# Performance work log

Measured on AMD Instinct MI355X. Metric: run time of the kernel, lower is better.

Reference implementation:

```python
import jax, jax.numpy as jnp
import numpy as np

N_HEAD = 16
RMS_EPS = 1.1920928955078125e-07  # torch F.rms_norm default eps = finfo(fp32).eps


def _rope_tables(seq_len, head_dim, dtype):
    steps = jnp.arange(seq_len, dtype=jnp.float32)
    rates = 10000.0 ** (-jnp.arange(0, head_dim, 2, dtype=jnp.float32) / head_dim)
    angles = jnp.outer(steps, rates)  # [S, D/2]
    return jnp.cos(angles).astype(dtype)[None, None], jnp.sin(angles).astype(dtype)[None, None]


def _apply_rotary(x, cos, sin):
    # interleaved RoPE: pairs (x[2i], x[2i+1]) rotated
    left = x[..., ::2]
    right = x[..., 1::2]
    lo = left * cos - right * sin
    ro = left * sin + right * cos
    return jnp.stack((lo, ro), axis=-1).reshape(x.shape)


def _rms_norm(x, eps=RMS_EPS):
    ms = jnp.mean(jnp.square(x), axis=-1, keepdims=True)
    return x * jax.lax.rsqrt(ms + eps)


def setup_inputs() -> dict:
    key = jax.random.key(0)
    k1, k2, k3 = jax.random.split(key, 3)
    B, S, E = 2, 2048, 2048
    x = jax.random.normal(k1, (B, S, E), dtype=jnp.float32)
    w_qkv = jax.random.normal(k2, (3 * E, E), dtype=jnp.float32) * (E ** -0.5)
    w_proj = jax.random.normal(k3, (E, E), dtype=jnp.float32) * (E ** -0.5)
    return {"x": x, "w_qkv": w_qkv, "w_proj": w_proj}


def reference(x, w_qkv, w_proj):
    B, S, E = x.shape
    H = N_HEAD
    D = E // H

    qkv = x @ w_qkv.T  # [B, S, 3E]
    q, k, v = jnp.split(qkv, 3, axis=-1)
    # [B, S, E] -> [B, H, S, D]
    q = q.reshape(B, S, H, D).transpose(0, 2, 1, 3)
    k = k.reshape(B, S, H, D).transpose(0, 2, 1, 3)
    v = v.reshape(B, S, H, D).transpose(0, 2, 1, 3)

    cos, sin = _rope_tables(S, D, x.dtype)  # [1,1,S,D/2]
    q = _apply_rotary(q, cos, sin)
    k = _apply_rotary(k, cos, sin)

    q = _rms_norm(q)
    k = _rms_norm(k)

    scale = 1.0 / jnp.sqrt(jnp.asarray(D, dtype=x.dtype))
    scores = jnp.einsum("bhqd,bhkd->bhqk", q, k) * scale  # [B,H,S,S]
    causal = jnp.tril(jnp.ones((S, S), dtype=bool))
    scores = jnp.where(causal[None, None], scores, jnp.asarray(-jnp.inf, dtype=scores.dtype))
    attn = jax.nn.softmax(scores, axis=-1)
    y = jnp.einsum("bhqk,bhkd->bhqd", attn, v)  # [B,H,S,D]
    y = y.transpose(0, 2, 1, 3).reshape(B, S, E)
    return y @ w_proj.T
```

## Files before the change

### kernel.cpp

```cpp
#include <hip/hip_runtime.h>

typedef unsigned short ushort_t;
using bf16x8 = __attribute__((ext_vector_type(8))) short;
using f32x4  = __attribute__((ext_vector_type(4))) float;

#define DEV static __device__ __forceinline__

DEV unsigned short f2bf(float f) {
  union { float f; unsigned u; } a; a.f = f;
  unsigned r = a.u + 0x7fffu + ((a.u >> 16) & 1u);
  return (unsigned short)(r >> 16);
}
DEV float bf2f(unsigned short u) {
  union { unsigned u; float f; } a; a.u = ((unsigned)u) << 16;
  return a.f;
}
DEV void load_lds16(const void* g, void* l) {
  __builtin_amdgcn_global_load_lds(
      (const __attribute__((address_space(1))) void*)g,
      (__attribute__((address_space(3))) void*)l, 16, 0, 0);
}

__global__ __launch_bounds__(256) void cast_kernel(
    const float* __restrict__ src, ushort_t* __restrict__ dst, int n4) {
  int i = blockIdx.x * 256 + threadIdx.x;
  if (i >= n4) return;
  float4 f = ((const float4*)src)[i];
  ushort4 o;
  o.x = f2bf(f.x); o.y = f2bf(f.y); o.z = f2bf(f.z); o.w = f2bf(f.w);
  ((ushort4*)dst)[i] = o;
}

__global__ __launch_bounds__(256) void rope_tables_kernel(float* __restrict__ tab) {
  int idx = blockIdx.x * 256 + threadIdx.x;
  int s = idx >> 6, i = idx & 63;
  float rate = exp2f(-13.287712379549449f * ((float)(2 * i) * (1.0f / 128.0f)));
  float ang = (float)s * rate;
  tab[idx * 2]     = cosf(ang);
  tab[idx * 2 + 1] = sinf(ang);
}

template<int BM, int BN, int OUTF32>
__global__ __launch_bounds__(256, 2) void gemm_bal(
    const ushort_t* __restrict__ A, const ushort_t* __restrict__ Bm,
    void* __restrict__ C, int M, int N, int K) {
  constexpr int MF   = BM / 32;
  constexpr int NF   = BN / 32;
  constexpr int NCA  = BM / 64;
  constexpr int NCB  = BN / 64;
  constexpr int NC   = NCA + NCB;
  constexpr int ABY  = BM * 64;
  constexpr int BUFB = (BM + BN) * 64;
  __shared__ __align__(16) char lds[2 * BUFB];

  const int nby = M / BM;
  const int nwg = nby * (N / BN);
  const int orig = blockIdx.x;
  const int wgid = (orig & 7) * (nwg >> 3) + (orig >> 3);
  const int bm = (wgid % nby) * BM;
  const int bn = (wgid / nby) * BN;

  const int tid = threadIdx.x;
  const int lane = tid & 63;
  const int wave = tid >> 6;
  const int ql = lane & 15, lk = lane >> 4;
  const int wm = wave >> 1, wn = wave & 1;

  f32x4 acc[MF][NF];
#pragma unroll
  for (int m = 0; m < MF; ++m)
#pragma unroll
    for (int n = 0; n < NF; ++n) acc[m][n] = (f32x4){0.f, 0.f, 0.f, 0.f};

  const int rin  = tid >> 2;
  const int sswz = ((tid & 3) ^ ((rin >> 1) & 3)) * 16;
  const size_t rb = (size_t)K * 2;
  const char* src[NC];
#pragma unroll
  for (int c = 0; c < NCA; ++c)
    src[c] = (const char*)A + (size_t)(bm + c * 64 + rin) * rb + sswz;
#pragma unroll
  for (int c = 0; c < NCB; ++c)
    src[NCA + c] = (const char*)Bm + (size_t)(bn + c * 64 + rin) * rb + sswz;
  char* const ldsc = (char*)lds;
  const int dT = tid * 16;

  int aOff[MF], bOff[NF];
#pragma unroll
  for (int m = 0; m < MF; ++m) {
    const int r = wm * (BM / 2) + m * 16 + ql;
    aOff[m] = r * 64 + ((lk ^ ((r >> 1) & 3)) * 16);
  }
#pragma unroll
  for (int n = 0; n < NF; ++n) {
    const int r = wn * (BN / 2) + n * 16 + ql;
    bOff[n] = ABY + r * 64 + ((lk ^ ((r >> 1) & 3)) * 16);
  }

#define STAGE(BB, KT) do {                                   \
    char* d_ = ldsc + (BB) * BUFB + dT;                      \
    const size_t ko_ = (size_t)(KT) * 64;                    \
    _Pragma("unroll")                                        \
    for (int c = 0; c < NC; ++c)                             \
      load_lds16(src[c] + ko_, d_ + c * 4096);               \
  } while (0)
#define MFMA(a, b, c) __builtin_amdgcn_mfma_f32_16x16x32_bf16(a, b, c, 0, 0, 0)

  const int ns = K >> 5;
  STAGE(0, 0);
  __syncthreads();

  for (int t = 0; t < ns; ++t) {
    const int nk = (t + 1 < ns) ? t + 1 : t;
    STAGE((t + 1) & 1, nk);
    const char* sb = ldsc + (t & 1) * BUFB;
    bf16x8 bF[NF], aF[MF];
#pragma unroll
    for (int n = 0; n < NF; ++n) bF[n] = *(const bf16x8*)(sb + bOff[n]);
#pragma unroll
    for (int m = 0; m < MF; ++m) aF[m] = *(const bf16x8*)(sb + aOff[m]);
    __builtin_amdgcn_s_setprio(1);
#pragma unroll
    for (int m = 0; m < MF; ++m)
#pragma unroll
      for (int n = 0; n < NF; ++n)
        acc[m][n] = MFMA(aF[m], bF[n], acc[m][n]);
    __builtin_amdgcn_s_setprio(0);
    __syncthreads();
  }
#undef STAGE
#undef MFMA

#pragma unroll
  for (int m = 0; m < MF; ++m)
#pragma unroll
    for (int i = 0; i < 4; ++i) {
      const size_t row = (size_t)(bm + wm * (BM / 2) + m * 16 + lk * 4 + i);
#pragma unroll
      for (int n = 0; n < NF; ++n) {
        const size_t col = (size_t)(bn + wn * (BN / 2) + n * 16 + ql);
        float v = acc[m][n][i];
        if (OUTF32) ((float*)C)[row * (size_t)N + col] = v;
        else        ((ushort_t*)C)[row * (size_t)N + col] = f2bf(v);
      }
    }
}

__global__ __launch_bounds__(256) void rope_rms_kernel(
    const ushort_t* __restrict__ qkv, ushort_t* __restrict__ q,
    ushort_t* __restrict__ k, ushort_t* __restrict__ vt,
    const float* __restrict__ tab) {
  const int lane = threadIdx.x & 63;
  const int row  = blockIdx.x * 4 + (threadIdx.x >> 6);
  const int h = row & 15;
  int t = row >> 4;
  const int which = t % 3; t /= 3;
  const int s = t & 2047;
  const int b = t >> 11;
  const size_t src = ((size_t)(b * 2048 + s)) * 6144 + which * 2048 + h * 128 + lane * 2;
  ushort2 xv = *(const ushort2*)&qkv[src];
  if (which == 2) {
    size_t vbase = ((size_t)((b * 16 + h) * 128 + lane * 2)) * 2048 + s;
    vt[vbase]        = xv.x;
    vt[vbase + 2048] = xv.y;
    return;
  }
  float lo = bf2f(xv.x), ro = bf2f(xv.y);
  const float2 cs = *(const float2*)&tab[(s * 64 + lane) * 2];
  float l2 = lo * cs.x - ro * cs.y;
  float r2 = lo * cs.y + ro * cs.x;
  float ss = l2 * l2 + r2 * r2;
#pragma unroll
  for (int off = 1; off < 64; off <<= 1) ss += __shfl_xor(ss, off);
  float inv = rsqrtf(ss * (1.0f / 128.0f) + 1.1920928955078125e-07f);
  if (which == 0) inv *= 0.1275174398f;
  lo = l2 * inv; ro = r2 * inv;
  ushort_t* dst = (which == 0) ? q : k;
  ushort2 o; o.x = f2bf(lo); o.y = f2bf(ro);
  *(ushort2*)&dst[(((size_t)(b * 16 + h)) * 2048 + s) * 128 + lane * 2] = o;
}

__global__ __launch_bounds__(256, 1) void attn_kernel(
    const ushort_t* __restrict__ Q, const ushort_t* __restrict__ K,
    const ushort_t* __restrict__ VT, ushort_t* __restrict__ Y) {
  __shared__ __align__(16) ushort_t sK[2][64 * 128];
  __shared__ __align__(16) ushort_t sV[2][128 * 64];
  const int bh = blockIdx.x;
  const int yp = blockIdx.y;
  const int wave = threadIdx.x >> 6, lane = threadIdx.x & 63;
  const int ql = lane & 15, lk = lane >> 4;
  const size_t hq = (size_t)bh * 2048 * 128;
  const int b = bh >> 4, h = bh & 15;

  const char* kB = (const char*)(K + hq);
  const char* vB = (const char*)(VT + hq);
  const char* kSrc[4]; char* kDst[4];
  const char* vSrc[4]; char* vDst[4];
#pragma unroll
  for (int t = 0; t < 4; ++t) {
    int r = wave * 16 + t * 4 + (lane >> 4);
    int kgr = r >> 4, lkr = (r >> 2) & 3, ir = r & 3;
    int rho = (kgr >> 1) * 32 + lkr * 8 + (kgr & 1) * 4 + ir;
    kSrc[t] = kB + rho * 256 + (((lane & 15) * 16) ^ ((r & 7) << 4));
    kDst[t] = (char*)sK + (wave * 256 + t * 64 + lane) * 16;
    int d = wave * 32 + t * 8 + (lane >> 3);
    vSrc[t] = vB + (size_t)d * 4096 + (((lane & 7) * 16) ^ ((d & 7) << 4));
    vDst[t] = (char*)sV + (wave * 256 + t * 64 + lane) * 16;
  }

#define STAGEKV(KT, BB) do {                                         \
    _Pragma("unroll")                                                \
    for (int t_ = 0; t_ < 4; ++t_) {                                 \
      load_lds16(kSrc[t_] + (size_t)(KT) * 16384, kDst[t_] + (BB) * 16384); \
      load_lds16(vSrc[t_] + (KT) * 128, vDst[t_] + (BB) * 16384);    \
    }                                                                \
  } while (0)

  int buf = 0;
  STAGEKV(0, 0);
  __syncthreads();

  for (int pass = 0; pass < 2; ++pass) {
    const int qt = pass ? (15 - yp) : yp;
    const int ktmax = 2 * qt + 1;
    const int q0 = qt * 128 + wave * 32 + ql;

    bf16x8 qf[2][4];
#pragma unroll
    for (int g = 0; g < 2; ++g)
#pragma unroll
      for (int ks = 0; ks < 4; ++ks)
        qf[g][ks] = *(const bf16x8*)&Q[hq + (size_t)(q0 + g * 16) * 128 + ks * 32 + lk * 8];

    f32x4 acc[2][8];
#pragma unroll
    for (int g = 0; g < 2; ++g)
#pragma unroll
      for (int dg = 0; dg < 8; ++dg) acc[g][dg] = (f32x4){0.f, 0.f, 0.f, 0.f};
    float mrow[2] = {-3.0e38f, -3.0e38f}, lsum[2] = {0.f, 0.f};

    for (int kt = 0; kt <= ktmax; ++kt) {
      const int nk = (kt < ktmax) ? kt + 1 : (pass == 0 ? 0 : ktmax);
      STAGEKV(nk, buf ^ 1);
      const char* sKb = (const char*)sK + buf * 16384;
      const char* sVb = (const char*)sV + buf * 16384;

      f32x4 st[2][4];
#pragma unroll
      for (int g = 0; g < 2; ++g)
#pragma unroll
        for (int kg = 0; kg < 4; ++kg) st[g][kg] = (f32x4){0.f, 0.f, 0.f, 0.f};
#pragma unroll
      for (int kg = 0; kg < 4; ++kg) {
        const int row = kg * 16 + ql;
        const int rswz = (row & 7) << 4;
#pragma unroll
        for (int ks = 0; ks < 4; ++ks) {
          bf16x8 kf = *(const bf16x8*)(sKb + row * 256 + ((ks * 64 + lk * 16) ^ rswz));
          st[0][kg] = __builtin_amdgcn_mfma_f32_16x16x32_bf16(kf, qf[0][ks], st[0][kg], 0, 0, 0);
          st[1][kg] = __builtin_amdgcn_mfma_f32_16x16x32_bf16(kf, qf[1][ks], st[1][kg], 0, 0, 0);
        }
      }
      bf16x8 pb[2][2];
#pragma unroll
      for (int g = 0; g < 2; ++g) {
        const int q = q0 + g * 16;
        float sv[4][4]; float mp = -3.0e38f;
#pragma unroll
        for (int kg = 0; kg < 4; ++kg) {
          const int kl = ((kg >> 1) << 5) + lk * 8 + ((kg & 1) << 2);
#pragma unroll
          for (int i = 0; i < 4; ++i) {
            const int key = kt * 64 + kl + i;
            float v = (key <= q) ? st[g][kg][i] : -3.0e38f;
            sv[kg][i] = v;
            mp = fmaxf(mp, v);
          }
        }
        mp = fmaxf(mp, __shfl_xor(mp, 16));
        mp = fmaxf(mp, __shfl_xor(mp, 32));
        const float mn = fmaxf(mrow[g], mp);
        const float corr = exp2f(mrow[g] - mn);
        mrow[g] = mn;
        float p[4][4]; float rs = 0.f;
#pragma unroll
        for (int kg = 0; kg < 4; ++kg)
#pragma unroll
          for (int i = 0; i < 4; ++i) {
            float e = exp2f(sv[kg][i] - mn);
            p[kg][i] = e; rs += e;
          }
        rs += __shfl_xor(rs, 16);
        rs += __shfl_xor(rs, 32);
        lsum[g] = lsum[g] * corr + rs;
#pragma unroll
        for (int dg = 0; dg < 8; ++dg)
#pragma unroll
          for (int i = 0; i < 4; ++i) acc[g][dg][i] *= corr;
#pragma unroll
        for (int c = 0; c < 2; ++c) {
          union { bf16x8 v; ushort_t u[8]; } pk;
#pragma unroll
          for (int j = 0; j < 8; ++j) pk.u[j] = f2bf(p[2 * c + (j >> 2)][j & 3]);
          pb[g][c] = pk.v;
        }
      }
#pragma unroll
      for (int dg = 0; dg < 8; ++dg) {
        const int d = dg * 16 + ql;
        const int dswz = (d & 7) << 4;
#pragma unroll
        for (int c = 0; c < 2; ++c) {
          bf16x8 vf = *(const bf16x8*)(sVb + d * 128 + ((c * 64 + lk * 16) ^ dswz));
          acc[0][dg] = __builtin_amdgcn_mfma_f32_16x16x32_bf16(vf, pb[0][c], acc[0][dg], 0, 0, 0);
          acc[1][dg] = __builtin_amdgcn_mfma_f32_16x16x32_bf16(vf, pb[1][c], acc[1][dg], 0, 0, 0);
        }
      }
      __syncthreads();
      buf ^= 1;
    }

#pragma unroll
    for (int g = 0; g < 2; ++g) {
      const float inv = 1.0f / lsum[g];
      const size_t orow = ((size_t)(b * 2048 + q0 + g * 16)) * 2048 + h * 128;
#pragma unroll
      for (int dg = 0; dg < 8; ++dg) {
        ushort4 o;
        o.x = f2bf(acc[g][dg][0] * inv);
        o.y = f2bf(acc[g][dg][1] * inv);
        o.z = f2bf(acc[g][dg][2] * inv);
        o.w = f2bf(acc[g][dg][3] * inv);
        *(ushort4*)&Y[orow + dg * 16 + lk * 4] = o;
      }
    }
  }
#undef STAGEKV
}

extern "C" void kernel_launch(void* const* d_in, const int* in_sizes, int n_in,
                              void* d_out, int out_size, void* d_ws, size_t ws_size,
                              hipStream_t stream) {
  const float* x     = (const float*)d_in[0];
  const float* wqkv  = (const float*)d_in[1];
  const float* wproj = (const float*)d_in[2];
  float* out = (float*)d_out;
  char* ws = (char*)d_ws;

  ushort_t* x_bf     = (ushort_t*)(ws);
  ushort_t* wqkv_bf  = (ushort_t*)(ws + 16777216);
  ushort_t* wproj_bf = (ushort_t*)(ws + 41943040);
  ushort_t* qkv_bf   = (ushort_t*)(ws + 50331648);
  ushort_t* q_bf     = (ushort_t*)(ws + 100663296);
  ushort_t* k_bf     = (ushort_t*)(ws + 117440512);
  ushort_t* vt_bf    = (ushort_t*)(ws + 134217728);
  float*    tab      = (float*)(ws + 150994944);
  if (ws_size < 152043520u) return;

  cast_kernel<<<8192, 256, 0, stream>>>(x, x_bf, 2097152);
  cast_kernel<<<12288, 256, 0, stream>>>(wqkv, wqkv_bf, 3145728);
  cast_kernel<<<4096, 256, 0, stream>>>(wproj, wproj_bf, 1048576);
  rope_tables_kernel<<<512, 256, 0, stream>>>(tab);

  gemm_bal<256, 128, 0><<<768, 256, 0, stream>>>(x_bf, wqkv_bf, qkv_bf, 4096, 6144, 2048);

  rope_rms_kernel<<<49152, 256, 0, stream>>>(qkv_bf, q_bf, k_bf, vt_bf, tab);

  attn_kernel<<<dim3(32, 8), 256, 0, stream>>>(q_bf, k_bf, vt_bf, qkv_bf );

  gemm_bal<128, 128, 1><<<512, 256, 0, stream>>>(qkv_bf, wproj_bf, out, 4096, 2048, 2048);
}
```

Measured before the change: 339.8 us.

## Merge cast kernels, enlarge GEMM tiles, restructure attention to 32-key tiles

Folds the three fp32-to-bf16 cast launches into one kernel. Raises GEMM tile sizes (256x256 for QKV, 256x128 for the output projection) and drops the two-blocks-per-CU launch bound. It also interleaves B-fragment loads with the MFMAs. The attention kernel now uses 32-key K/V tiles with a single pass per block, 512 blocks ordered longest causal tile first, and two blocks per CU. The intent is fewer launches, more reuse per tile and better occupancy and load balance in attention, at the cost of higher register pressure in the GEMMs and more loop iterations per attention block.

```diff
diff --git a/kernel.cpp b/kernel.cpp
--- a/kernel.cpp
+++ b/kernel.cpp
@@ -21,14 +21,19 @@
       (__attribute__((address_space(3))) void*)l, 16, 0, 0);
 }
 
-__global__ __launch_bounds__(256) void cast_kernel(
-    const float* __restrict__ src, ushort_t* __restrict__ dst, int n4) {
+__global__ __launch_bounds__(256) void cast3_kernel(
+    const float* __restrict__ x, const float* __restrict__ wqkv,
+    const float* __restrict__ wproj, ushort_t* __restrict__ xb,
+    ushort_t* __restrict__ qb, ushort_t* __restrict__ pb) {
   int i = blockIdx.x * 256 + threadIdx.x;
-  if (i >= n4) return;
-  float4 f = ((const float4*)src)[i];
+  const float4* s; ushort4* d; int off;
+  if (i < 2097152)      { s = (const float4*)x;     d = (ushort4*)xb; off = i; }
+  else if (i < 5242880) { s = (const float4*)wqkv;  d = (ushort4*)qb; off = i - 2097152; }
+  else                  { s = (const float4*)wproj; d = (ushort4*)pb; off = i - 5242880; }
+  float4 f = s[off];
   ushort4 o;
   o.x = f2bf(f.x); o.y = f2bf(f.y); o.z = f2bf(f.z); o.w = f2bf(f.w);
-  ((ushort4*)dst)[i] = o;
+  d[off] = o;
 }
 
 __global__ __launch_bounds__(256) void rope_tables_kernel(float* __restrict__ tab) {
@@ -41,14 +46,13 @@
 }
 
 template<int BM, int BN, int OUTF32>
-__global__ __launch_bounds__(256, 2) void gemm_bal(
+__global__ __launch_bounds__(256) void gemm_mega(
     const ushort_t* __restrict__ A, const ushort_t* __restrict__ Bm,
     void* __restrict__ C, int M, int N, int K) {
   constexpr int MF   = BM / 32;
   constexpr int NF   = BN / 32;
   constexpr int NCA  = BM / 64;
-  constexpr int NCB  = BN / 64;
-  constexpr int NC   = NCA + NCB;
+  constexpr int NC   = (BM + BN) / 64;
   constexpr int ABY  = BM * 64;
   constexpr int BUFB = (BM + BN) * 64;
   __shared__ __align__(16) char lds[2 * BUFB];
@@ -60,7 +64,7 @@
   const int bm = (wgid % nby) * BM;
   const int bn = (wgid / nby) * BN;
 
-  const int tid = threadIdx.x;
+  const int tid  = threadIdx.x;
   const int lane = tid & 63;
   const int wave = tid >> 6;
   const int ql = lane & 15, lk = lane >> 4;
@@ -77,11 +81,10 @@
   const size_t rb = (size_t)K * 2;
   const char* src[NC];
 #pragma unroll
-  for (int c = 0; c < NCA; ++c)
-    src[c] = (const char*)A + (size_t)(bm + c * 64 + rin) * rb + sswz;
-#pragma unroll
-  for (int c = 0; c < NCB; ++c)
-    src[NCA + c] = (const char*)Bm + (size_t)(bn + c * 64 + rin) * rb + sswz;
+  for (int c = 0; c < NC; ++c) {
+    if (c < NCA) src[c] = (const char*)A  + (size_t)(bm + c * 64 + rin) * rb + sswz;
+    else         src[c] = (const char*)Bm + (size_t)(bn + (c - NCA) * 64 + rin) * rb + sswz;
+  }
   char* const ldsc = (char*)lds;
   const int dT = tid * 16;
 
@@ -114,17 +117,17 @@
     const int nk = (t + 1 < ns) ? t + 1 : t;
     STAGE((t + 1) & 1, nk);
     const char* sb = ldsc + (t & 1) * BUFB;
-    bf16x8 bF[NF], aF[MF];
-#pragma unroll
-    for (int n = 0; n < NF; ++n) bF[n] = *(const bf16x8*)(sb + bOff[n]);
+    bf16x8 aF[MF];
 #pragma unroll
     for (int m = 0; m < MF; ++m) aF[m] = *(const bf16x8*)(sb + aOff[m]);
     __builtin_amdgcn_s_setprio(1);
 #pragma unroll
-    for (int m = 0; m < MF; ++m)
-#pragma unroll
-      for (int n = 0; n < NF; ++n)
-        acc[m][n] = MFMA(aF[m], bF[n], acc[m][n]);
+    for (int n = 0; n < NF; ++n) {
+      bf16x8 bF = *(const bf16x8*)(sb + bOff[n]);
+#pragma unroll
+      for (int m = 0; m < MF; ++m)
+        acc[m][n] = MFMA(aF[m], bF, acc[m][n]);
+    }
     __builtin_amdgcn_s_setprio(0);
     __syncthreads();
   }
@@ -180,162 +183,153 @@
   *(ushort2*)&dst[(((size_t)(b * 16 + h)) * 2048 + s) * 128 + lane * 2] = o;
 }
 
-__global__ __launch_bounds__(256, 1) void attn_kernel(
+__global__ __launch_bounds__(256, 2) void attn_kernel(
     const ushort_t* __restrict__ Q, const ushort_t* __restrict__ K,
     const ushort_t* __restrict__ VT, ushort_t* __restrict__ Y) {
-  __shared__ __align__(16) ushort_t sK[2][64 * 128];
-  __shared__ __align__(16) ushort_t sV[2][128 * 64];
-  const int bh = blockIdx.x;
-  const int yp = blockIdx.y;
-  const int wave = threadIdx.x >> 6, lane = threadIdx.x & 63;
+  __shared__ __align__(16) ushort_t sK[2 * 32 * 128];
+  __shared__ __align__(16) ushort_t sV[2 * 128 * 32];
+  const int gx = blockIdx.x;
+  const int bh = gx & 31;
+  const int qt = (gx < 256) ? (15 - (gx >> 5)) : ((gx - 256) >> 5);
+  const int tid = threadIdx.x;
+  const int wave = tid >> 6, lane = tid & 63;
   const int ql = lane & 15, lk = lane >> 4;
   const size_t hq = (size_t)bh * 2048 * 128;
   const int b = bh >> 4, h = bh & 15;
 
   const char* kB = (const char*)(K + hq);
   const char* vB = (const char*)(VT + hq);
-  const char* kSrc[4]; char* kDst[4];
-  const char* vSrc[4]; char* vDst[4];
-#pragma unroll
-  for (int t = 0; t < 4; ++t) {
-    int r = wave * 16 + t * 4 + (lane >> 4);
-    int kgr = r >> 4, lkr = (r >> 2) & 3, ir = r & 3;
-    int rho = (kgr >> 1) * 32 + lkr * 8 + (kgr & 1) * 4 + ir;
-    kSrc[t] = kB + rho * 256 + (((lane & 15) * 16) ^ ((r & 7) << 4));
-    kDst[t] = (char*)sK + (wave * 256 + t * 64 + lane) * 16;
-    int d = wave * 32 + t * 8 + (lane >> 3);
-    vSrc[t] = vB + (size_t)d * 4096 + (((lane & 7) * 16) ^ ((d & 7) << 4));
-    vDst[t] = (char*)sV + (wave * 256 + t * 64 + lane) * 16;
-  }
-
-#define STAGEKV(KT, BB) do {                                         \
-    _Pragma("unroll")                                                \
-    for (int t_ = 0; t_ < 4; ++t_) {                                 \
-      load_lds16(kSrc[t_] + (size_t)(KT) * 16384, kDst[t_] + (BB) * 16384); \
-      load_lds16(vSrc[t_] + (KT) * 128, vDst[t_] + (BB) * 16384);    \
-    }                                                                \
+  const char* kSrc[2]; const char* vSrc[2];
+#pragma unroll
+  for (int c = 0; c < 2; ++c) {
+    const int r = c * 16 + (tid >> 4);
+    const int rho = ((r >> 2) & 3) * 8 + ((r >> 4) & 1) * 4 + (r & 3);
+    kSrc[c] = kB + rho * 256 + (((tid & 15) ^ (r & 7)) * 16);
+    const int d = c * 64 + (tid >> 2);
+    vSrc[c] = vB + (size_t)d * 4096 + (((tid & 3) ^ ((d >> 1) & 3)) * 16);
+  }
+  char* const sKc = (char*)sK;
+  char* const sVc = (char*)sV;
+  const int dT = tid * 16;
+
+#define STAGEKV(KT, BB) do {                                              \
+    _Pragma("unroll")                                                     \
+    for (int c_ = 0; c_ < 2; ++c_) {                                      \
+      load_lds16(kSrc[c_] + (size_t)(KT) * 8192, sKc + (BB) * 8192 + c_ * 4096 + dT); \
+      load_lds16(vSrc[c_] + (KT) * 64,           sVc + (BB) * 8192 + c_ * 4096 + dT); \
+    }                                                                     \
   } while (0)
-
-  int buf = 0;
+#define MFMA(a, b, c) __builtin_amdgcn_mfma_f32_16x16x32_bf16(a, b, c, 0, 0, 0)
+
+  const int ktmax = 4 * qt + 3;
+  const int q0 = qt * 128 + wave * 32 + ql;
+
+  bf16x8 qf[2][4];
+#pragma unroll
+  for (int g = 0; g < 2; ++g)
+#pragma unroll
+    for (int ks = 0; ks < 4; ++ks)
+      qf[g][ks] = *(const bf16x8*)&Q[hq + (size_t)(q0 + g * 16) * 128 + ks * 32 + lk * 8];
+
+  f32x4 acc[2][8];
+#pragma unroll
+  for (int g = 0; g < 2; ++g)
+#pragma unroll
+    for (int dg = 0; dg < 8; ++dg) acc[g][dg] = (f32x4){0.f, 0.f, 0.f, 0.f};
+  float mrow[2] = {-3.0e38f, -3.0e38f}, lsum[2] = {0.f, 0.f};
+
   STAGEKV(0, 0);
   __syncthreads();
-
-  for (int pass = 0; pass < 2; ++pass) {
-    const int qt = pass ? (15 - yp) : yp;
-    const int ktmax = 2 * qt + 1;
-    const int q0 = qt * 128 + wave * 32 + ql;
-
-    bf16x8 qf[2][4];
-#pragma unroll
-    for (int g = 0; g < 2; ++g)
-#pragma unroll
-      for (int ks = 0; ks < 4; ++ks)
-        qf[g][ks] = *(const bf16x8*)&Q[hq + (size_t)(q0 + g * 16) * 128 + ks * 32 + lk * 8];
-
-    f32x4 acc[2][8];
-#pragma unroll
-    for (int g = 0; g < 2; ++g)
-#pragma unroll
-      for (int dg = 0; dg < 8; ++dg) acc[g][dg] = (f32x4){0.f, 0.f, 0.f, 0.f};
-    float mrow[2] = {-3.0e38f, -3.0e38f}, lsum[2] = {0.f, 0.f};
-
-    for (int kt = 0; kt <= ktmax; ++kt) {
-      const int nk = (kt < ktmax) ? kt + 1 : (pass == 0 ? 0 : ktmax);
-      STAGEKV(nk, buf ^ 1);
-      const char* sKb = (const char*)sK + buf * 16384;
-      const char* sVb = (const char*)sV + buf * 16384;
-
-      f32x4 st[2][4];
-#pragma unroll
-      for (int g = 0; g < 2; ++g)
-#pragma unroll
-        for (int kg = 0; kg < 4; ++kg) st[g][kg] = (f32x4){0.f, 0.f, 0.f, 0.f};
-#pragma unroll
-      for (int kg = 0; kg < 4; ++kg) {
-        const int row = kg * 16 + ql;
-        const int rswz = (row & 7) << 4;
-#pragma unroll
-        for (int ks = 0; ks < 4; ++ks) {
-          bf16x8 kf = *(const bf16x8*)(sKb + row * 256 + ((ks * 64 + lk * 16) ^ rswz));
-          st[0][kg] = __builtin_amdgcn_mfma_f32_16x16x32_bf16(kf, qf[0][ks], st[0][kg], 0, 0, 0);
-          st[1][kg] = __builtin_amdgcn_mfma_f32_16x16x32_bf16(kf, qf[1][ks], st[1][kg], 0, 0, 0);
+  int buf = 0;
+
+  for (int kt = 0; kt <= ktmax; ++kt) {
+    const int nk = (kt < ktmax) ? kt + 1 : kt;
+    STAGEKV(nk, buf ^ 1);
+    const char* sKb = sKc + buf * 8192;
+    const char* sVb = sVc + buf * 8192;
+
+    f32x4 st[2][2];
+#pragma unroll
+    for (int g = 0; g < 2; ++g) { st[g][0] = (f32x4){0.f,0.f,0.f,0.f}; st[g][1] = (f32x4){0.f,0.f,0.f,0.f}; }
+#pragma unroll
+    for (int kg = 0; kg < 2; ++kg) {
+      const int row = kg * 16 + ql;
+      const int rswz = (row & 7) << 4;
+#pragma unroll
+      for (int ks = 0; ks < 4; ++ks) {
+        bf16x8 kf = *(const bf16x8*)(sKb + row * 256 + ((ks * 64 + lk * 16) ^ rswz));
+        st[0][kg] = MFMA(kf, qf[0][ks], st[0][kg]);
+        st[1][kg] = MFMA(kf, qf[1][ks], st[1][kg]);
+      }
+    }
+    bf16x8 pb[2];
+#pragma unroll
+    for (int g = 0; g < 2; ++g) {
+      const int q = q0 + g * 16;
+      float sv[2][4]; float mp = -3.0e38f;
+#pragma unroll
+      for (int kg = 0; kg < 2; ++kg) {
+        const int kl = lk * 8 + kg * 4;
+#pragma unroll
+        for (int i = 0; i < 4; ++i) {
+          const int key = kt * 32 + kl + i;
+          float v = (key <= q) ? st[g][kg][i] : -3.0e38f;
+          sv[kg][i] = v;
+          mp = fmaxf(mp, v);
         }
       }
-      bf16x8 pb[2][2];
-#pragma unroll
-      for (int g = 0; g < 2; ++g) {
-        const int q = q0 + g * 16;
-        float sv[4][4]; float mp = -3.0e38f;
-#pragma unroll
-        for (int kg = 0; kg < 4; ++kg) {
-          const int kl = ((kg >> 1) << 5) + lk * 8 + ((kg & 1) << 2);
-#pragma unroll
-          for (int i = 0; i < 4; ++i) {
-            const int key = kt * 64 + kl + i;
-            float v = (key <= q) ? st[g][kg][i] : -3.0e38f;
-            sv[kg][i] = v;
-            mp = fmaxf(mp, v);
-          }
+      mp = fmaxf(mp, __shfl_xor(mp, 16));
+      mp = fmaxf(mp, __shfl_xor(mp, 32));
+      const float mn = fmaxf(mrow[g], mp);
+      const float corr = exp2f(mrow[g] - mn);
+      mrow[g] = mn;
+      float p[2][4]; float rs = 0.f;
+#pragma unroll
+      for (int kg = 0; kg < 2; ++kg)
+#pragma unroll
+        for (int i = 0; i < 4; ++i) {
+          float e = exp2f(sv[kg][i] - mn);
+          p[kg][i] = e; rs += e;
         }
-        mp = fmaxf(mp, __shfl_xor(mp, 16));
-        mp = fmaxf(mp, __shfl_xor(mp, 32));
-        const float mn = fmaxf(mrow[g], mp);
-        const float corr = exp2f(mrow[g] - mn);
-        mrow[g] = mn;
-        float p[4][4]; float rs = 0.f;
-#pragma unroll
-        for (int kg = 0; kg < 4; ++kg)
-#pragma unroll
-          for (int i = 0; i < 4; ++i) {
-            float e = exp2f(sv[kg][i] - mn);
-            p[kg][i] = e; rs += e;
-          }
-        rs += __shfl_xor(rs, 16);
-        rs += __shfl_xor(rs, 32);
-        lsum[g] = lsum[g] * corr + rs;
-#pragma unroll
-        for (int dg = 0; dg < 8; ++dg)
-#pragma unroll
-          for (int i = 0; i < 4; ++i) acc[g][dg][i] *= corr;
-#pragma unroll
-        for (int c = 0; c < 2; ++c) {
-          union { bf16x8 v; ushort_t u[8]; } pk;
-#pragma unroll
-          for (int j = 0; j < 8; ++j) pk.u[j] = f2bf(p[2 * c + (j >> 2)][j & 3]);
-          pb[g][c] = pk.v;
-        }
-      }
-#pragma unroll
-      for (int dg = 0; dg < 8; ++dg) {
-        const int d = dg * 16 + ql;
-        const int dswz = (d & 7) << 4;
-#pragma unroll
-        for (int c = 0; c < 2; ++c) {
-          bf16x8 vf = *(const bf16x8*)(sVb + d * 128 + ((c * 64 + lk * 16) ^ dswz));
-          acc[0][dg] = __builtin_amdgcn_mfma_f32_16x16x32_bf16(vf, pb[0][c], acc[0][dg], 0, 0, 0);
-          acc[1][dg] = __builtin_amdgcn_mfma_f32_16x16x32_bf16(vf, pb[1][c], acc[1][dg], 0, 0, 0);
-        }
-      }
-      __syncthreads();
-      buf ^= 1;
-    }
-
-#pragma unroll
-    for (int g = 0; g < 2; ++g) {
-      const float inv = 1.0f / lsum[g];
-      const size_t orow = ((size_t)(b * 2048 + q0 + g * 16)) * 2048 + h * 128;
-#pragma unroll
-      for (int dg = 0; dg < 8; ++dg) {
-        ushort4 o;
-        o.x = f2bf(acc[g][dg][0] * inv);
-        o.y = f2bf(acc[g][dg][1] * inv);
-        o.z = f2bf(acc[g][dg][2] * inv);
-        o.w = f2bf(acc[g][dg][3] * inv);
-        *(ushort4*)&Y[orow + dg * 16 + lk * 4] = o;
-      }
+      rs += __shfl_xor(rs, 16);
+      rs += __shfl_xor(rs, 32);
+      lsum[g] = lsum[g] * corr + rs;
+#pragma unroll
+      for (int dg = 0; dg < 8; ++dg)
+#pragma unroll
+        for (int i = 0; i < 4; ++i) acc[g][dg][i] *= corr;
+      union { bf16x8 v; ushort_t u[8]; } pk;
+#pragma unroll
+      for (int j = 0; j < 8; ++j) pk.u[j] = f2bf(p[j >> 2][j & 3]);
+      pb[g] = pk.v;
+    }
+#pragma unroll
+    for (int dg = 0; dg < 8; ++dg) {
+      const int d = dg * 16 + ql;
+      bf16x8 vf = *(const bf16x8*)(sVb + d * 64 + ((lk ^ ((d >> 1) & 3)) * 16));
+      acc[0][dg] = MFMA(vf, pb[0], acc[0][dg]);
+      acc[1][dg] = MFMA(vf, pb[1], acc[1][dg]);
+    }
+    __syncthreads();
+    buf ^= 1;
+  }
+
+#pragma unroll
+  for (int g = 0; g < 2; ++g) {
+    const float inv = 1.0f / lsum[g];
+    const size_t orow = ((size_t)(b * 2048 + q0 + g * 16)) * 2048 + h * 128;
+#pragma unroll
+    for (int dg = 0; dg < 8; ++dg) {
+      ushort4 o;
+      o.x = f2bf(acc[g][dg][0] * inv);
+      o.y = f2bf(acc[g][dg][1] * inv);
+      o.z = f2bf(acc[g][dg][2] * inv);
+      o.w = f2bf(acc[g][dg][3] * inv);
+      *(ushort4*)&Y[orow + dg * 16 + lk * 4] = o;
     }
   }
 #undef STAGEKV
+#undef MFMA
 }
 
 extern "C" void kernel_launch(void* const* d_in, const int* in_sizes, int n_in,
@@ -357,16 +351,14 @@
   float*    tab      = (float*)(ws + 150994944);
   if (ws_size < 152043520u) return;
 
-  cast_kernel<<<8192, 256, 0, stream>>>(x, x_bf, 2097152);
-  cast_kernel<<<12288, 256, 0, stream>>>(wqkv, wqkv_bf, 3145728);
-  cast_kernel<<<4096, 256, 0, stream>>>(wproj, wproj_bf, 1048576);
+  cast3_kernel<<<24576, 256, 0, stream>>>(x, wqkv, wproj, x_bf, wqkv_bf, wproj_bf);
   rope_tables_kernel<<<512, 256, 0, stream>>>(tab);
 
-  gemm_bal<256, 128, 0><<<768, 256, 0, stream>>>(x_bf, wqkv_bf, qkv_bf, 4096, 6144, 2048);
+  gemm_mega<256, 256, 0><<<384, 256, 0, stream>>>(x_bf, wqkv_bf, qkv_bf, 4096, 6144, 2048);
 
   rope_rms_kernel<<<49152, 256, 0, stream>>>(qkv_bf, q_bf, k_bf, vt_bf, tab);
 
-  attn_kernel<<<dim3(32, 8), 256, 0, stream>>>(q_bf, k_bf, vt_bf, qkv_bf );
-
-  gemm_bal<128, 128, 1><<<512, 256, 0, stream>>>(qkv_bf, wproj_bf, out, 4096, 2048, 2048);
-}
+  attn_kernel<<<512, 256, 0, stream>>>(q_bf, k_bf, vt_bf, qkv_bf );
+
+  gemm_mega<256, 128, 1><<<256, 256, 0, stream>>>(qkv_bf, wproj_bf, out, 4096, 2048, 2048);
+}
```

Measured after the change: 391.3 us. 15.2% more time.
